# Performance work log

Hardware: AMD Instinct MI355X
Metric: run time of the kernel (lower is better)

The kernel has to match this reference:

```python
import jax, jax.numpy as jnp
import numpy as np

B, N = 16, 512            # graphs, atoms per graph
F_DIM, H, D = 128, 64, 16  # feature_dim, hidden_dim, far_source_dim
CUT, GROWTH = 5.0, 2.0
NS, NT = 3, 2
MULT = GROWTH ** NS        # default far_max_radius_multiplier = 8
EMAX = CUT * MULT          # 40.0
TOT = NS + NT              # 5 shells total
SF = D + 3                 # 19 per-shell features
SE_IN = TOT * SF           # 95
EH_IN = 4 * D + SE_IN      # 159
N_RBF = 8
BOUNDS = [(5.0, 10.0), (10.0, 20.0), (20.0, 40.0), (40.0, 80.0), (80.0, float('inf'))]


def ln(x, g, b):
    m = x.mean(-1, keepdims=True)
    v = x.var(-1, keepdims=True)
    return (x - m) / jnp.sqrt(v + 1e-5) * g + b


def setup_inputs() -> dict:
    key = jax.random.key(0)
    ks = jax.random.split(key, 16)
    W = lambda k, i, o: jax.random.normal(k, (i, o), jnp.float32) / np.sqrt(i)
    inp = {}
    inp['x'] = jax.random.normal(ks[0], (B * N, F_DIM), jnp.float32)
    inp['pos'] = jax.random.uniform(ks[1], (B * N, 3), jnp.float32) * 80.0
    inp['batch'] = jnp.repeat(jnp.arange(B, dtype=jnp.int32), N)
    inp['num_graphs'] = B
    inp['in_ln_g'] = jnp.ones(F_DIM); inp['in_ln_b'] = jnp.zeros(F_DIM)
    inp['src_w1'] = W(ks[2], F_DIM, H); inp['src_b1'] = jnp.zeros(H)
    inp['src_w2'] = W(ks[3], H, D);     inp['src_b2'] = jnp.zeros(D)
    inp['src_ln_g'] = jnp.ones(D); inp['src_ln_b'] = jnp.zeros(D)
    inp['se_ln_g'] = jnp.ones(SE_IN); inp['se_ln_b'] = jnp.zeros(SE_IN)
    inp['se_w1'] = W(ks[4], SE_IN, H); inp['se_b1'] = jnp.zeros(H)
    inp['se_w2'] = W(ks[5], H, D);     inp['se_b2'] = jnp.zeros(D)
    inp['eh_ln_g'] = jnp.ones(EH_IN); inp['eh_ln_b'] = jnp.zeros(EH_IN)
    inp['eh_w1'] = W(ks[6], EH_IN, H); inp['eh_b1'] = jnp.zeros(H)
    inp['eh_w2'] = W(ks[7], H, 1);     inp['eh_b2'] = jnp.zeros(1)
    inp['k_screen'] = jnp.float32(-8.0)
    inp['kg_w1'] = W(ks[8], N_RBF + 2, 32); inp['kg_b1'] = jnp.zeros(32)
    inp['kg_w2'] = jnp.zeros((32, 1)); inp['kg_b2'] = jnp.zeros(1)  # zero-init per source
    inp['far_gate'] = jnp.float32(0.2)
    inp['energy_scale'] = jnp.float32(0.0)
    return inp


def reference(x, pos, batch, num_graphs, in_ln_g, in_ln_b, src_w1, src_b1, src_w2, src_b2,
              src_ln_g, src_ln_b, se_ln_g, se_ln_b, se_w1, se_b1, se_w2, se_b2,
              eh_ln_g, eh_ln_b, eh_w1, eh_b1, eh_w2, eh_b2,
              k_screen, kg_w1, kg_b1, kg_w2, kg_b2, far_gate, energy_scale):
    M = x.shape[0]
    n = M // num_graphs
    # per-atom source features
    h = ln(x, in_ln_g, in_ln_b)
    src = jax.nn.silu(h @ src_w1 + src_b1) @ src_w2 + src_b2
    src = ln(src, src_ln_g, src_ln_b)
    # graph-wise neutralization (subtract per-graph mean)
    gsum = jax.ops.segment_sum(src, batch, num_segments=num_graphs)
    cnt = jax.ops.segment_sum(jnp.ones((M, 1), x.dtype), batch, num_segments=num_graphs)
    src = src - (gsum / jnp.maximum(cnt, 1.0))[batch]
    # pairwise distances per graph
    p = pos.reshape(num_graphs, n, 3)
    s = src.reshape(num_graphs, n, D)
    diff = p[:, :, None, :] - p[:, None, :, :]
    d = jnp.sqrt((diff * diff).sum(-1) + 1e-12)  # [B,n,n]
    not_self = ~jnp.eye(n, dtype=bool)[None]
    # physical kernel with learned RBF gate
    screening = jax.nn.softplus(k_screen)
    base = jnp.exp(-screening * d) / jnp.maximum(d, 1e-6)
    centers = jnp.linspace(CUT, EMAX, N_RBF)
    spacing = (EMAX - CUT) / (N_RBF - 1)
    gamma = 1.0 / (spacing * spacing)
    dc = d[..., None]
    rbf = jnp.exp(-gamma * (dc - centers) ** 2)
    gin = jnp.concatenate([dc / CUT, dc / EMAX, rbf], -1)
    gate = 1.0 + jnp.tanh(jax.nn.silu(gin @ kg_w1 + kg_b1) @ kg_w2 + kg_b2)[..., 0]
    ker = base * gate
    # shell statistics: kernel-weighted mean source, count, mean_r, rms_r per shell
    feats = []
    for lo, up in BOUNDS:
        m = (d >= lo) & not_self
        if np.isfinite(up):
            m = m & (d < up)
        mf = m.astype(x.dtype)
        c = mf.sum(-1)
        denom = jnp.maximum(c, 1.0)
        mean = jnp.einsum('bij,bjc->bic', ker * mf, s) / denom[..., None]
        mr = (mf * d).sum(-1) / denom
        rr = jnp.sqrt((mf * d * d).sum(-1) / denom + 1e-12)
        feats.append(jnp.concatenate([mean, c[..., None], mr[..., None], rr[..., None]], -1))
    shell = jnp.concatenate(feats, -1).reshape(M, SE_IN)  # [M, 95]
    emb = jax.nn.silu(ln(shell, se_ln_g, se_ln_b) @ se_w1 + se_b1) @ se_w2 + se_b2
    ein = jnp.concatenate([src, emb, src * emb, src - emb, shell], -1)  # [M, 159]
    pa = (jax.nn.silu(ln(ein, eh_ln_g, eh_ln_b) @ eh_w1 + eh_b1) @ eh_w2 + eh_b2)[..., 0]
    pa = pa * jnp.tanh(far_gate) * jnp.exp(energy_scale)
    return jax.ops.segment_sum(pa, batch, num_segments=num_graphs)  # per-graph energies [B]
```

## Files before the change

### kernel.cpp

```cpp
#include <hip/hip_runtime.h>
#include <hip/hip_bf16.h>
#include <math.h>

#define B_G   16
#define N_A   512
#define M_AT  8192
#define FD    128
#define HD    64
#define DD    16
#define SEIN  95
#define EHIN  159
#define NLUT  512
#define DMAXF 140.0f

__device__ __forceinline__ float silu_f(float z) { return z / (1.f + __expf(-z)); }

__global__ __launch_bounds__(128) void k_front(
    const float* __restrict__ x,
    const float* __restrict__ g, const float* __restrict__ bb,
    const float* __restrict__ w1, const float* __restrict__ b1,
    const float* __restrict__ w2, const float* __restrict__ b2,
    const float* __restrict__ lng, const float* __restrict__ lnb,
    const float* __restrict__ k_screen,
    const float* __restrict__ kg_w1, const float* __restrict__ kg_b1,
    const float* __restrict__ kg_w2, const float* __restrict__ kg_b2,
    float* __restrict__ srcout, float* __restrict__ partials,
    float2* __restrict__ lut, float* __restrict__ out) {
  int t = threadIdx.x;

  __shared__ __align__(16) float xns[2][FD][5];
  __shared__ __align__(16) float hb[2][HD][5];
  __shared__ float psum[2][16];
  __shared__ float w1l[320], b1l[32], w2l[32];

  if (blockIdx.x >= 1024) {
    int lb = blockIdx.x - 1024;
    if (lb == 0 && t < B_G) out[t] = 0.f;
    for (int idx = t; idx < 320; idx += 128) w1l[idx] = kg_w1[idx];
    if (t < 32) { b1l[t] = kg_b1[t]; w2l[t] = kg_w2[t]; }
    __syncthreads();
    int i = lb * 128 + t;
    float step = DMAXF / (float)(NLUT - 1);
    float ksv = k_screen[0];
    float screening = fmaxf(ksv, 0.f) + log1pf(expf(-fabsf(ksv)));
    float b2v = kg_b2[0];
    float vals[2];
#pragma unroll
    for (int e = 0; e < 2; ++e) {
      int ii = min(i + e, NLUT - 1);
      float d = (float)ii * step;
      float base = expf(-screening * d) / fmaxf(d, 1e-6f);
      float gin[10];
      gin[0] = d * (1.f / 5.0f);
      gin[1] = d * (1.f / 40.0f);
#pragma unroll
      for (int kk = 0; kk < 8; ++kk) {
        float u = d - (5.0f + 5.0f * (float)kk);
        gin[2 + kk] = expf(-(1.f / 25.f) * u * u);
      }
      float accv = 0.f;
      for (int h = 0; h < 32; ++h) {
        float z = b1l[h];
#pragma unroll
        for (int kk = 0; kk < 10; ++kk) z += gin[kk] * w1l[kk * 32 + h];
        accv += silu_f(z) * w2l[h];
      }
      vals[e] = base * (1.f + tanhf(accv + b2v));
    }
    lut[i] = make_float2(vals[0], vals[1] - vals[0]);
    return;
  }

  int wave = t >> 6, lane = t & 63;
  int a = lane >> 4;
  int s = lane & 15;
  int aBase = blockIdx.x * 8 + wave * 4;

  float xr[8];
  {
    const float4* xp = (const float4*)(x + (size_t)(aBase + a) * FD + s * 8);
    float4 v0 = xp[0], v1 = xp[1];
    xr[0]=v0.x; xr[1]=v0.y; xr[2]=v0.z; xr[3]=v0.w;
    xr[4]=v1.x; xr[5]=v1.y; xr[6]=v1.z; xr[7]=v1.w;
  }
  float sm_ = 0.f;
#pragma unroll
  for (int i = 0; i < 8; ++i) sm_ += xr[i];
  sm_ += __shfl_xor(sm_, 1); sm_ += __shfl_xor(sm_, 2);
  sm_ += __shfl_xor(sm_, 4); sm_ += __shfl_xor(sm_, 8);
  float m = sm_ * (1.f / 128.f);
  float v2 = 0.f;
#pragma unroll
  for (int i = 0; i < 8; ++i) { float d = xr[i] - m; v2 += d * d; }
  v2 += __shfl_xor(v2, 1); v2 += __shfl_xor(v2, 2);
  v2 += __shfl_xor(v2, 4); v2 += __shfl_xor(v2, 8);
  float inv = rsqrtf(v2 * (1.f / 128.f) + 1e-5f);
#pragma unroll
  for (int i = 0; i < 8; ++i) {
    int k = s * 8 + i;
    xns[wave][k][a] = (xr[i] - m) * inv * g[k] + bb[k];
  }

  float acc[4] = {0.f, 0.f, 0.f, 0.f};
#pragma unroll 8
  for (int k = 0; k < FD; ++k) {
    float4 wv = ((const float4*)(w1 + (size_t)k * HD))[s];
    float xa = xns[wave][k][a];
    acc[0] += wv.x * xa; acc[1] += wv.y * xa;
    acc[2] += wv.z * xa; acc[3] += wv.w * xa;
  }
  {
    float4 bv = ((const float4*)b1)[s];
    hb[wave][s * 4 + 0][a] = silu_f(acc[0] + bv.x);
    hb[wave][s * 4 + 1][a] = silu_f(acc[1] + bv.y);
    hb[wave][s * 4 + 2][a] = silu_f(acc[2] + bv.z);
    hb[wave][s * 4 + 3][a] = silu_f(acc[3] + bv.w);
  }

  float e = 0.f;
#pragma unroll 8
  for (int k = 0; k < HD; ++k) e += hb[wave][k][a] * w2[k * DD + s];
  float val = e + b2[s];

  float smv = val;
  smv += __shfl_xor(smv, 1); smv += __shfl_xor(smv, 2);
  smv += __shfl_xor(smv, 4); smv += __shfl_xor(smv, 8);
  float mm = smv * (1.f / 16.f);
  float dv = val - mm;
  float vv = dv * dv;
  vv += __shfl_xor(vv, 1); vv += __shfl_xor(vv, 2);
  vv += __shfl_xor(vv, 4); vv += __shfl_xor(vv, 8);
  float iv = rsqrtf(vv * (1.f / 16.f) + 1e-5f);
  float ov = dv * iv * lng[s] + lnb[s];
  srcout[(size_t)(aBase + a) * DD + s] = ov;

  float lsum = ov;
  lsum += __shfl_xor(lsum, 16); lsum += __shfl_xor(lsum, 32);
  if (lane < 16) psum[wave][lane] = lsum;
  __syncthreads();
  if (t < 16) partials[(size_t)blockIdx.x * 16 + t] = psum[0][t] + psum[1][t];
}

__global__ __launch_bounds__(256) void k_pairs_tail(
    const float* __restrict__ pos, const float* __restrict__ src,
    const float2* __restrict__ lut, const float* __restrict__ partials,
    const float* __restrict__ se_ln_g, const float* __restrict__ se_ln_b,
    const float* __restrict__ se_w1, const float* __restrict__ se_b1,
    const float* __restrict__ se_w2, const float* __restrict__ se_b2,
    const float* __restrict__ eh_ln_g, const float* __restrict__ eh_ln_b,
    const float* __restrict__ eh_w1, const float* __restrict__ eh_b1,
    const float* __restrict__ eh_w2, const float* __restrict__ eh_b2,
    const float* __restrict__ far_gate, const float* __restrict__ energy_scale,
    float* __restrict__ out) {
  int gph = blockIdx.x >> 7;
  int blk = blockIdx.x & 127;
  int t = threadIdx.x, wave = t >> 6, lane = t & 63;
  int i_local = blk * 4 + wave;

  __shared__ __align__(16) float sp[N_A * 3];
  __shared__ __align__(16) float ss[N_A * DD];
  __shared__ __align__(16) float2 luts[NLUT];
  __shared__ __align__(16) float wb[4][N_A];
  __shared__ unsigned char tbs[4][N_A];
  __shared__ float smean[16];
  __shared__ __align__(16) float einL[4][160];
  __shared__ __align__(16) float shnL[4][96];
  __shared__ __align__(16) float hbL[4][64];
  __shared__ float redv[4];

  for (int idx = t; idx < N_A * 3 / 4; idx += 256)
    ((float4*)sp)[idx] = ((const float4*)(pos + (size_t)gph * N_A * 3))[idx];
  for (int idx = t; idx < N_A * DD / 4; idx += 256)
    ((float4*)ss)[idx] = ((const float4*)(src + (size_t)gph * N_A * DD))[idx];
  if (t < NLUT / 2) ((float4*)luts)[t] = ((const float4*)lut)[t];
  if (t < 64) {
    int c = t & 15, grp = t >> 4;
    float sm = 0.f;
#pragma unroll
    for (int kk = 0; kk < 16; ++kk)
      sm += partials[(size_t)(gph * 64 + grp * 16 + kk) * 16 + c];
    sm += __shfl_xor(sm, 16); sm += __shfl_xor(sm, 32);
    if (t < 16) smean[c] = sm * (1.f / 512.f);
  }
  __syncthreads();

  float px = sp[i_local * 3], py = sp[i_local * 3 + 1], pz = sp[i_local * 3 + 2];
  float cnt[5] = {0,0,0,0,0}, sdv[5] = {0,0,0,0,0}, sdd[5] = {0,0,0,0,0}, swq[5] = {0,0,0,0,0};
  const float lscale = (float)(NLUT - 1) / DMAXF;

#pragma unroll
  for (int it = 0; it < 8; ++it) {
    int jv = lane + it * 64;
    float dx = px - sp[jv * 3], dy = py - sp[jv * 3 + 1], dz = pz - sp[jv * 3 + 2];
    float d2 = dx * dx + dy * dy + dz * dz + 1e-12f;
    float d = sqrtf(d2);
    bool valid = (jv != i_local) && (d >= 5.0f);
    int tq = (d >= 10.f) + (d >= 20.f) + (d >= 40.f) + (d >= 80.f);
    float xq = d * lscale;
    int i0 = min((int)xq, NLUT - 2);
    float f = xq - (float)i0;
    float2 L = luts[i0];
    float w = valid ? (L.x + L.y * f) : 0.f;
    wb[wave][jv] = w;
    tbs[wave][jv] = (unsigned char)tq;
    float dm = valid ? d : 0.f;
    float ddm = valid ? d * d : 0.f;
    float cm = valid ? 1.f : 0.f;
#pragma unroll
    for (int q = 0; q < 5; ++q) {
      bool mq = (tq == q);
      cnt[q] += mq ? cm : 0.f;
      sdv[q] += mq ? dm : 0.f;
      sdd[q] += mq ? ddm : 0.f;
      swq[q] += mq ? w : 0.f;
    }
  }
#pragma unroll
  for (int q = 0; q < 5; ++q) {
#pragma unroll
    for (int o = 32; o > 0; o >>= 1) {
      cnt[q] += __shfl_xor(cnt[q], o);
      sdv[q] += __shfl_xor(sdv[q], o);
      sdd[q] += __shfl_xor(sdd[q], o);
      swq[q] += __shfl_xor(swq[q], o);
    }
  }
  __syncthreads();

  int jlow = lane & 15, cq = lane >> 4;
  float accq[5][4] = {};
  {
    const float* ssb = &ss[jlow * DD + cq * 4];
    const float* wbb = &wb[wave][jlow];
    const unsigned char* tbb = &tbs[wave][jlow];
#pragma unroll
    for (int jj = 0; jj < 32; ++jj) {
      float4 sv = *(const float4*)(ssb + jj * 256);
      float w = wbb[jj * 16];
      int tq = tbb[jj * 16];
      float w0 = (tq == 0) ? w : 0.f;
      float w1_ = (tq == 1) ? w : 0.f;
      float w2_ = (tq == 2) ? w : 0.f;
      float w3_ = (tq == 3) ? w : 0.f;
      float w4_ = (tq == 4) ? w : 0.f;
      accq[0][0] += w0 * sv.x; accq[0][1] += w0 * sv.y; accq[0][2] += w0 * sv.z; accq[0][3] += w0 * sv.w;
      accq[1][0] += w1_ * sv.x; accq[1][1] += w1_ * sv.y; accq[1][2] += w1_ * sv.z; accq[1][3] += w1_ * sv.w;
      accq[2][0] += w2_ * sv.x; accq[2][1] += w2_ * sv.y; accq[2][2] += w2_ * sv.z; accq[2][3] += w2_ * sv.w;
      accq[3][0] += w3_ * sv.x; accq[3][1] += w3_ * sv.y; accq[3][2] += w3_ * sv.z; accq[3][3] += w3_ * sv.w;
      accq[4][0] += w4_ * sv.x; accq[4][1] += w4_ * sv.y; accq[4][2] += w4_ * sv.z; accq[4][3] += w4_ * sv.w;
    }
  }
#pragma unroll
  for (int q = 0; q < 5; ++q)
#pragma unroll
    for (int i = 0; i < 4; ++i) {
      float v = accq[q][i];
      v += __shfl_xor(v, 1); v += __shfl_xor(v, 2);
      v += __shfl_xor(v, 4); v += __shfl_xor(v, 8);
      accq[q][i] = v;
    }

  if (jlow == 0) {
#pragma unroll
    for (int q = 0; q < 5; ++q) {
      float denom = fmaxf(cnt[q], 1.f);
#pragma unroll
      for (int i = 0; i < 4; ++i) {
        int c = cq * 4 + i;
        einL[wave][64 + q * 19 + c] = (accq[q][i] - smean[c] * swq[q]) / denom;
      }
    }
  }
  if (lane < 5) {
    int q = lane;
    float denom = fmaxf(cnt[q], 1.f);
    einL[wave][64 + q * 19 + 16] = cnt[q];
    einL[wave][64 + q * 19 + 17] = sdv[q] / denom;
    einL[wave][64 + q * 19 + 18] = sqrtf(sdd[q] / denom + 1e-12f);
  }

  {
    float v0 = einL[wave][64 + lane];
    float v1 = (lane < 31) ? einL[wave][128 + lane] : 0.f;
    float s1 = v0 + v1;
#pragma unroll
    for (int o = 32; o > 0; o >>= 1) s1 += __shfl_xor(s1, o);
    float mn = s1 * (1.f / (float)SEIN);
    float d0 = v0 - mn, d1 = (lane < 31) ? v1 - mn : 0.f;
    float sq = d0 * d0 + d1 * d1;
#pragma unroll
    for (int o = 32; o > 0; o >>= 1) sq += __shfl_xor(sq, o);
    float invv = rsqrtf(sq * (1.f / (float)SEIN) + 1e-5f);
    shnL[wave][lane] = d0 * invv * se_ln_g[lane] + se_ln_b[lane];
    if (lane < 31)
      shnL[wave][64 + lane] = d1 * invv * se_ln_g[64 + lane] + se_ln_b[64 + lane];
  }

  {
    float z = se_b1[lane];
#pragma unroll 5
    for (int k = 0; k < SEIN; ++k) z += shnL[wave][k] * se_w1[(size_t)k * HD + lane];
    hbL[wave][lane] = silu_f(z);
  }

  {
    int c = lane & 15, kq = lane >> 4;
    float e = 0.f;
#pragma unroll
    for (int i = 0; i < 16; ++i) {
      int k = kq * 16 + i;
      e += hbL[wave][k] * se_w2[k * DD + c];
    }
    e += __shfl_down(e, 32);
    e += __shfl_down(e, 16);
    if (lane < 16) {
      float ev = e + se_b2[lane];
      float svv = ss[i_local * DD + lane] - smean[lane];
      einL[wave][lane] = svv;
      einL[wave][16 + lane] = ev;
      einL[wave][32 + lane] = svv * ev;
      einL[wave][48 + lane] = svv - ev;
    }
  }

  {
    float u0 = einL[wave][lane];
    float u1 = einL[wave][64 + lane];
    float u2 = (lane < 31) ? einL[wave][128 + lane] : 0.f;
    float s1 = u0 + u1 + u2;
#pragma unroll
    for (int o = 32; o > 0; o >>= 1) s1 += __shfl_xor(s1, o);
    float mn = s1 * (1.f / (float)EHIN);
    float e0 = u0 - mn, e1 = u1 - mn, e2 = (lane < 31) ? u2 - mn : 0.f;
    float sq = e0 * e0 + e1 * e1 + e2 * e2;
#pragma unroll
    for (int o = 32; o > 0; o >>= 1) sq += __shfl_xor(sq, o);
    float invv = rsqrtf(sq * (1.f / (float)EHIN) + 1e-5f);
    einL[wave][lane] = e0 * invv * eh_ln_g[lane] + eh_ln_b[lane];
    einL[wave][64 + lane] = e1 * invv * eh_ln_g[64 + lane] + eh_ln_b[64 + lane];
    if (lane < 31)
      einL[wave][128 + lane] = e2 * invv * eh_ln_g[128 + lane] + eh_ln_b[128 + lane];
  }

  {
    float z2 = eh_b1[lane];
#pragma unroll 3
    for (int k = 0; k < EHIN; ++k) z2 += einL[wave][k] * eh_w1[(size_t)k * HD + lane];
    float pa = silu_f(z2) * eh_w2[lane];
#pragma unroll
    for (int o = 32; o > 0; o >>= 1) pa += __shfl_xor(pa, o);
    if (lane == 0) redv[wave] = pa + eh_b2[0];
  }
  __syncthreads();
  if (t == 0) {
    float tot = redv[0] + redv[1] + redv[2] + redv[3];
    atomicAdd(&out[gph], tot * tanhf(far_gate[0]) * expf(energy_scale[0]));
  }
}

extern "C" void kernel_launch(void* const* d_in, const int* in_sizes, int n_in,
                              void* d_out, int out_size, void* d_ws, size_t ws_size,
                              hipStream_t stream) {
  const float* x         = (const float*)d_in[0];
  const float* pos       = (const float*)d_in[1];
  const float* in_ln_g   = (const float*)d_in[4];
  const float* in_ln_b   = (const float*)d_in[5];
  const float* src_w1    = (const float*)d_in[6];
  const float* src_b1    = (const float*)d_in[7];
  const float* src_w2    = (const float*)d_in[8];
  const float* src_b2    = (const float*)d_in[9];
  const float* src_ln_g  = (const float*)d_in[10];
  const float* src_ln_b  = (const float*)d_in[11];
  const float* se_ln_g   = (const float*)d_in[12];
  const float* se_ln_b   = (const float*)d_in[13];
  const float* se_w1     = (const float*)d_in[14];
  const float* se_b1     = (const float*)d_in[15];
  const float* se_w2     = (const float*)d_in[16];
  const float* se_b2     = (const float*)d_in[17];
  const float* eh_ln_g   = (const float*)d_in[18];
  const float* eh_ln_b   = (const float*)d_in[19];
  const float* eh_w1     = (const float*)d_in[20];
  const float* eh_b1     = (const float*)d_in[21];
  const float* eh_w2     = (const float*)d_in[22];
  const float* eh_b2     = (const float*)d_in[23];
  const float* k_screen  = (const float*)d_in[24];
  const float* kg_w1     = (const float*)d_in[25];
  const float* kg_b1     = (const float*)d_in[26];
  const float* kg_w2     = (const float*)d_in[27];
  const float* kg_b2     = (const float*)d_in[28];
  const float* far_gate  = (const float*)d_in[29];
  const float* en_scale  = (const float*)d_in[30];
  float* out = (float*)d_out;

  float* ws_src   = (float*)d_ws;
  float* ws_part  = ws_src + (size_t)M_AT * DD;
  float2* ws_lut  = (float2*)(ws_part + 1024 * 16);

  k_front<<<1028, 128, 0, stream>>>(x, in_ln_g, in_ln_b, src_w1, src_b1,
                                    src_w2, src_b2, src_ln_g, src_ln_b,
                                    k_screen, kg_w1, kg_b1, kg_w2, kg_b2,
                                    ws_src, ws_part, ws_lut, out);
  k_pairs_tail<<<B_G * (N_A / 4), 256, 0, stream>>>(
      pos, ws_src, ws_lut, ws_part,
      se_ln_g, se_ln_b, se_w1, se_b1, se_w2, se_b2,
      eh_ln_g, eh_ln_b, eh_w1, eh_b1, eh_w2, eh_b2,
      far_gate, en_scale, out);
}
```

Measured before the change: 230.0 us.

## Stage MLP weights into a reused shared-memory union buffer per block

The separate LDS arrays for positions, sources, the LUT and the per-wave weight and shell buffers are merged into one union buffer. Once the pair phase is done, the block reuses that space to cooperatively load se_w1/se_w2, and later eh_w1, so the four waves read weights from LDS instead of each streaming them from global memory. The atom's own source row is hoisted into a register before the buffer is overwritten. The cost is extra __syncthreads barriers and a full weight copy per block, even though each block handles only four atoms.

After: 218.8 us. 1.05x faster.

```diff
diff --git a/kernel.cpp b/kernel.cpp
--- a/kernel.cpp
+++ b/kernel.cpp
@@ -157,22 +157,24 @@
   int t = threadIdx.x, wave = t >> 6, lane = t & 63;
   int i_local = blk * 4 + wave;
 
-  __shared__ __align__(16) float sp[N_A * 3];
-  __shared__ __align__(16) float ss[N_A * DD];
-  __shared__ __align__(16) float2 luts[NLUT];
-  __shared__ __align__(16) float wb[4][N_A];
-  __shared__ unsigned char tbs[4][N_A];
-  __shared__ float smean[16];
+  __shared__ __align__(16) float bigU[13312];
   __shared__ __align__(16) float einL[4][160];
   __shared__ __align__(16) float shnL[4][96];
   __shared__ __align__(16) float hbL[4][64];
+  __shared__ float smean[16];
   __shared__ float redv[4];
+
+  float* sp = bigU;
+  float* ss = bigU + 1536;
+  float* wb = bigU + 9728;
+  unsigned char* tbs = (unsigned char*)(bigU + 11776);
+  float2* luts = (float2*)(bigU + 12288);
 
   for (int idx = t; idx < N_A * 3 / 4; idx += 256)
     ((float4*)sp)[idx] = ((const float4*)(pos + (size_t)gph * N_A * 3))[idx];
   for (int idx = t; idx < N_A * DD / 4; idx += 256)
     ((float4*)ss)[idx] = ((const float4*)(src + (size_t)gph * N_A * DD))[idx];
-  if (t < NLUT / 2) ((float4*)luts)[t] = ((const float4*)lut)[t];
+  ((float4*)luts)[t] = ((const float4*)lut)[t];
   if (t < 64) {
     int c = t & 15, grp = t >> 4;
     float sm = 0.f;
@@ -183,6 +185,8 @@
     if (t < 16) smean[c] = sm * (1.f / 512.f);
   }
   __syncthreads();
+
+  float sv_own = ss[i_local * DD + (lane & 15)];
 
   float px = sp[i_local * 3], py = sp[i_local * 3 + 1], pz = sp[i_local * 3 + 2];
   float cnt[5] = {0,0,0,0,0}, sdv[5] = {0,0,0,0,0}, sdd[5] = {0,0,0,0,0}, swq[5] = {0,0,0,0,0};
@@ -201,8 +205,8 @@
     float f = xq - (float)i0;
     float2 L = luts[i0];
     float w = valid ? (L.x + L.y * f) : 0.f;
-    wb[wave][jv] = w;
-    tbs[wave][jv] = (unsigned char)tq;
+    wb[wave * N_A + jv] = w;
+    tbs[wave * N_A + jv] = (unsigned char)tq;
     float dm = valid ? d : 0.f;
     float ddm = valid ? d * d : 0.f;
     float cm = valid ? 1.f : 0.f;
@@ -230,9 +234,9 @@
   int jlow = lane & 15, cq = lane >> 4;
   float accq[5][4] = {};
   {
-    const float* ssb = &ss[jlow * DD + cq * 4];
-    const float* wbb = &wb[wave][jlow];
-    const unsigned char* tbb = &tbs[wave][jlow];
+    const float* ssb = ss + jlow * DD + cq * 4;
+    const float* wbb = wb + wave * N_A + jlow;
+    const unsigned char* tbb = tbs + wave * N_A + jlow;
 #pragma unroll
     for (int jj = 0; jj < 32; ++jj) {
       float4 sv = *(const float4*)(ssb + jj * 256);
@@ -279,6 +283,13 @@
     einL[wave][64 + q * 19 + 18] = sqrtf(sdd[q] / denom + 1e-12f);
   }
 
+  __syncthreads();
+
+  for (int idx = t; idx < (SEIN * HD) / 4; idx += 256)
+    ((float4*)bigU)[idx] = ((const float4*)se_w1)[idx];
+  ((float4*)(bigU + SEIN * HD))[t] = ((const float4*)se_w2)[t];
+  __syncthreads();
+
   {
     float v0 = einL[wave][64 + lane];
     float v1 = (lane < 31) ? einL[wave][128 + lane] : 0.f;
@@ -298,30 +309,36 @@
 
   {
     float z = se_b1[lane];
-#pragma unroll 5
-    for (int k = 0; k < SEIN; ++k) z += shnL[wave][k] * se_w1[(size_t)k * HD + lane];
+#pragma unroll 8
+    for (int k = 0; k < SEIN; ++k) z += shnL[wave][k] * bigU[k * HD + lane];
     hbL[wave][lane] = silu_f(z);
   }
 
   {
     int c = lane & 15, kq = lane >> 4;
+    const float* w2s = bigU + SEIN * HD;
     float e = 0.f;
 #pragma unroll
     for (int i = 0; i < 16; ++i) {
       int k = kq * 16 + i;
-      e += hbL[wave][k] * se_w2[k * DD + c];
+      e += hbL[wave][k] * w2s[k * DD + c];
     }
     e += __shfl_down(e, 32);
     e += __shfl_down(e, 16);
     if (lane < 16) {
       float ev = e + se_b2[lane];
-      float svv = ss[i_local * DD + lane] - smean[lane];
+      float svv = sv_own - smean[lane];
       einL[wave][lane] = svv;
       einL[wave][16 + lane] = ev;
       einL[wave][32 + lane] = svv * ev;
       einL[wave][48 + lane] = svv - ev;
     }
   }
+
+  __syncthreads();
+  for (int idx = t; idx < (EHIN * HD) / 4; idx += 256)
+    ((float4*)bigU)[idx] = ((const float4*)eh_w1)[idx];
+  __syncthreads();
 
   {
     float u0 = einL[wave][lane];
@@ -344,8 +361,8 @@
 
   {
     float z2 = eh_b1[lane];
-#pragma unroll 3
-    for (int k = 0; k < EHIN; ++k) z2 += einL[wave][k] * eh_w1[(size_t)k * HD + lane];
+#pragma unroll 8
+    for (int k = 0; k < EHIN; ++k) z2 += einL[wave][k] * bigU[k * HD + lane];
     float pa = silu_f(z2) * eh_w2[lane];
 #pragma unroll
     for (int o = 32; o > 0; o >>= 1) pa += __shfl_xor(pa, o);
```
